# Optimization experiments

Hardware: AMD Instinct MI355X
Metric: run time of the kernel (lower is better)

## Reference

```python
import jax, jax.numpy as jnp
import numpy as np

EMBED = 1024
HEADS = 16
HEAD_DIM = EMBED // HEADS


def setup_inputs() -> dict:
    key = jax.random.key(0)
    ks = jax.random.split(key, 12)
    B, S, E = 2, 2048, EMBED
    scale = 1.0 / np.sqrt(E)
    inp = {
        "query": jax.random.normal(ks[0], (B, S, E), jnp.float32),
        "key": jax.random.normal(ks[1], (B, S, E), jnp.float32),
        "value": jax.random.normal(ks[2], (B, S, E), jnp.float32),
        "Wq": jax.random.normal(ks[3], (E, E), jnp.float32) * scale,
        "bq": jax.random.normal(ks[4], (E,), jnp.float32) * 0.01,
        "Wk": jax.random.normal(ks[5], (E, E), jnp.float32) * scale,
        "bk": jax.random.normal(ks[6], (E,), jnp.float32) * 0.01,
        "Wv": jax.random.normal(ks[7], (E, E), jnp.float32) * scale,
        "bv": jax.random.normal(ks[8], (E,), jnp.float32) * 0.01,
        "Wo": jax.random.normal(ks[9], (E, E), jnp.float32) * scale,
        "bo": jax.random.normal(ks[10], (E,), jnp.float32) * 0.01,
    }
    return inp


def reference(query, key, value, Wq, bq, Wk, bk, Wv, bv, Wo, bo):
    B, Sq, E = query.shape
    Sk = key.shape[1]
    H, D = HEADS, HEAD_DIM
    # QKV projections (torch Linear: x @ W.T + b)
    q = (query @ Wq.T + bq).reshape(B, Sq, H, D)
    k = (key @ Wk.T + bk).reshape(B, Sk, H, D)
    v = (value @ Wv.T + bv).reshape(B, Sk, H, D)
    # energy: [B, H, Sq, Sk]; note scale = 1/sqrt(embed_size), not head_dim
    energy = jnp.einsum("bqhd,bkhd->bhqk", q, k)
    scale = jnp.asarray(E, energy.dtype) ** 0.5
    attn = jax.nn.softmax(energy / scale, axis=-1)
    out = jnp.einsum("bhqk,bkhd->bqhd", attn, v).reshape(B, Sq, E)
    # fc_out (dropout is identity at eval)
    return out @ Wo.T + bo
```

## Files before the change

kernel.cpp:

```cpp
#include <hip/hip_runtime.h>
#include <hip/hip_bf16.h>

typedef __hip_bfloat16 bf16;
typedef short frag8 __attribute__((ext_vector_type(8)));
typedef _Float16 half4 __attribute__((ext_vector_type(4)));
typedef __fp16 fp16x2 __attribute__((ext_vector_type(2)));
typedef float f32x4 __attribute__((ext_vector_type(4)));

typedef __attribute__((address_space(3))) void lds_void;
typedef __attribute__((address_space(1))) const void gbl_void;

__device__ __forceinline__ void gld16(const void* g, void* l) {
  __builtin_amdgcn_global_load_lds((gbl_void*)g, (lds_void*)l, 16, 0, 0);
}

__device__ __forceinline__ unsigned short f2bf(float f) {
  union { float f; unsigned u; } x; x.f = f;
  unsigned r = x.u + 0x7FFFu + ((x.u >> 16) & 1u);
  return (unsigned short)(r >> 16);
}

#define QSCALE 0.0450842200278f
#define MFIX 4.0f

struct CvtArgs {
  const float4* src[7];
  ushort4* dst[7];
  int n4[7];
};
__global__ __launch_bounds__(256) void cvt_all(CvtArgs a) {
  const int t = blockIdx.y;
  const int i = blockIdx.x * 256 + threadIdx.x;
  if (i >= a.n4[t]) return;
  float4 v = a.src[t][i];
  ushort4 o;
  o.x = f2bf(v.x); o.y = f2bf(v.y); o.z = f2bf(v.z); o.w = f2bf(v.w);
  a.dst[t][i] = o;
}

template<int J0>
__device__ __forceinline__ void mfma16(f32x4 (&acc)[8][4], const frag8 (&af)[8], const frag8 (&bf2)[2]) {
  __builtin_amdgcn_s_setprio(1);
  #pragma unroll
  for (int i = 0; i < 8; ++i) {
    #pragma unroll
    for (int j = 0; j < 2; ++j)
      acc[i][J0 + j] = __builtin_amdgcn_mfma_f32_16x16x32_bf16(af[i], bf2[j], acc[i][J0 + j], 0, 0, 0);
  }
  __builtin_amdgcn_s_setprio(0);
}

__global__ __launch_bounds__(512, 2)
void gemm_qkv256(const bf16* __restrict__ A0, const bf16* __restrict__ A1, const bf16* __restrict__ A2,
                 const bf16* __restrict__ W0, const bf16* __restrict__ W1, const bf16* __restrict__ W2,
                 const float* __restrict__ b0, const float* __restrict__ b1, const float* __restrict__ b2,
                 void* __restrict__ o0, void* __restrict__ o1, void* __restrict__ o2) {
  __shared__ __align__(16) bf16 As[2][16384];
  __shared__ __align__(16) bf16 Bs[2][16384];
  const int tid = threadIdx.x;
  const int wave = tid >> 6, lane = tid & 63, quad = lane >> 4, l16 = lane & 15;
  const int wm = wave >> 2, wn = wave & 3;
  const int bn = blockIdx.x, bm = blockIdx.y, z = blockIdx.z;

  const bf16* A = A0; const bf16* W = W0; const float* bias = b0; void* out = o0;
  if (z == 1) { A = A1; W = W1; bias = b1; out = o1; }
  else if (z == 2) { A = A2; W = W2; bias = b2; out = o2; }

  const bf16* Ab = A + (size_t)bm * 256 * 1024;
  const bf16* Wb = W + (size_t)bn * 256 * 1024;
  const int c0_ = tid & 3, r0_ = tid >> 2;
  const int gcp = ((c0_ ^ ((r0_ >> 1) & 3)) << 3);
  const int rc2 = (quad ^ ((l16 >> 1) & 3)) << 3;

  auto stage = [&](const bf16* src, int kt, int kh, bf16* dst) {
    #pragma unroll
    for (int is = 0; is < 2; ++is) {
      const int r = r0_ + is * 128;
      gld16(src + (size_t)r * 1024 + kt * 64 + kh * 32 + gcp,
            (void*)(dst + (is * 512 + tid) * 8));
    }
  };
  auto ldsA = [&](const bf16* ah, frag8 (&af)[8]) {
    #pragma unroll
    for (int i = 0; i < 8; ++i)
      af[i] = *(const frag8*)&ah[(wm * 128 + i * 16 + l16) * 32 + rc2];
  };
  auto ldsB2 = [&](const bf16* bh, int j0, frag8 (&bf2)[2]) {
    #pragma unroll
    for (int j = 0; j < 2; ++j)
      bf2[j] = *(const frag8*)&bh[(wn * 64 + (j0 + j) * 16 + l16) * 32 + rc2];
  };

  f32x4 acc[8][4];
  #pragma unroll
  for (int i = 0; i < 8; ++i)
    #pragma unroll
    for (int j = 0; j < 4; ++j)
      acc[i][j] = (f32x4){0.f, 0.f, 0.f, 0.f};

  stage(Ab, 0, 0, &As[0][0]);
  stage(Wb, 0, 0, &Bs[0][0]);
  stage(Ab, 0, 1, &As[0][8192]);
  stage(Wb, 0, 1, &Bs[0][8192]);
  asm volatile("s_waitcnt vmcnt(0)" ::: "memory");
  __builtin_amdgcn_s_barrier();

  #pragma unroll 2
  for (int t = 0; t < 15; ++t) {
    const int buf = t & 1, nb = buf ^ 1;
    const bf16* a0 = &As[buf][0];    const bf16* a1 = &As[buf][8192];
    const bf16* b0 = &Bs[buf][0];    const bf16* b1 = &Bs[buf][8192];
    frag8 af[8], bf2[2];

    ldsA(a0, af); ldsB2(b0, 0, bf2);
    stage(Ab, t + 1, 0, &As[nb][0]);
    __builtin_amdgcn_s_barrier();
    asm volatile("s_waitcnt lgkmcnt(0)" ::: "memory");
    mfma16<0>(acc, af, bf2);
    __builtin_amdgcn_s_barrier();

    ldsB2(b0, 2, bf2);
    stage(Wb, t + 1, 0, &Bs[nb][0]);
    asm volatile("s_waitcnt vmcnt(4)" ::: "memory");
    __builtin_amdgcn_s_barrier();
    asm volatile("s_waitcnt lgkmcnt(0)" ::: "memory");
    mfma16<2>(acc, af, bf2);
    __builtin_amdgcn_s_barrier();

    ldsA(a1, af); ldsB2(b1, 0, bf2);
    stage(Ab, t + 1, 1, &As[nb][8192]);
    __builtin_amdgcn_s_barrier();
    asm volatile("s_waitcnt lgkmcnt(0)" ::: "memory");
    mfma16<0>(acc, af, bf2);
    __builtin_amdgcn_s_barrier();

    ldsB2(b1, 2, bf2);
    stage(Wb, t + 1, 1, &Bs[nb][8192]);
    asm volatile("s_waitcnt vmcnt(4)" ::: "memory");
    __builtin_amdgcn_s_barrier();
    asm volatile("s_waitcnt lgkmcnt(0)" ::: "memory");
    mfma16<2>(acc, af, bf2);
    __builtin_amdgcn_s_barrier();
  }

  {
    const bf16* a0 = &As[1][0];    const bf16* a1 = &As[1][8192];
    const bf16* b0 = &Bs[1][0];    const bf16* b1 = &Bs[1][8192];
    frag8 af[8], bf2[2];
    ldsA(a0, af); ldsB2(b0, 0, bf2);
    __builtin_amdgcn_s_barrier();
    asm volatile("s_waitcnt lgkmcnt(0)" ::: "memory");
    mfma16<0>(acc, af, bf2);
    ldsB2(b0, 2, bf2);
    asm volatile("s_waitcnt vmcnt(0)" ::: "memory");
    __builtin_amdgcn_s_barrier();
    asm volatile("s_waitcnt lgkmcnt(0)" ::: "memory");
    mfma16<2>(acc, af, bf2);
    ldsA(a1, af); ldsB2(b1, 0, bf2);
    asm volatile("s_waitcnt lgkmcnt(0)" ::: "memory");
    mfma16<0>(acc, af, bf2);
    ldsB2(b1, 2, bf2);
    asm volatile("s_waitcnt lgkmcnt(0)" ::: "memory");
    mfma16<2>(acc, af, bf2);
  }

  #pragma unroll
  for (int j = 0; j < 4; ++j) {
    const int col = bn * 256 + wn * 64 + j * 16 + l16;
    const float bv = bias[col];
    #pragma unroll
    for (int i = 0; i < 8; ++i) {
      #pragma unroll
      for (int r = 0; r < 4; ++r) {
        const int row = bm * 256 + wm * 128 + i * 16 + quad * 4 + r;
        float v = acc[i][j][r] + bv;
        const int b = row >> 11, s = row & 2047;
        const int hh = col >> 6, d = col & 63;
        const size_t bh = (size_t)(b * 16 + hh);
        if (z == 0) {
          v *= QSCALE;
          ((bf16*)out)[(bh * 2048 + s) * 64 + d] = __float2bfloat16(v);
        } else if (z == 1) {
          const int rr = s & 127;
          const size_t addr = bh * 131072 + (size_t)(s >> 7) * 8192 + (size_t)rr * 64
                            + (size_t)(((d >> 3) ^ (rr & 7)) << 3) + (d & 7);
          ((bf16*)out)[addr] = __float2bfloat16(v);
        } else {
          const int kvl = s & 127;
          const size_t addr = bh * 131072 + (size_t)(s >> 7) * 8192 + (size_t)d * 128
                            + (size_t)((((kvl >> 2) ^ (d & 15)) << 2)) + (kvl & 3);
          ((_Float16*)out)[addr] = (_Float16)v;
        }
      }
    }
  }
}

template<int MODE>
__global__ __launch_bounds__(256)
void gemm_bt(const bf16* __restrict__ A0, const bf16* __restrict__ A1, const bf16* __restrict__ A2,
             const bf16* __restrict__ W0, const bf16* __restrict__ W1, const bf16* __restrict__ W2,
             const float* __restrict__ b0, const float* __restrict__ b1, const float* __restrict__ b2,
             void* __restrict__ o0, void* __restrict__ o1, void* __restrict__ o2) {
  constexpr int NK = 1024;
  constexpr int BN = (MODE == 1) ? 128 : 64;
  __shared__ __align__(16) bf16 As[2][128 * 32];
  __shared__ __align__(16) bf16 Bs[2][BN * 32];
  const int tid = threadIdx.x;
  const int wave = tid >> 6, lane = tid & 63, quad = lane >> 4, l16 = lane & 15;
  const int wm = wave >> 1, wn = wave & 1;
  const int bn = blockIdx.x, bm = blockIdx.y;

  const bf16* A = A0; const bf16* W = W0; const float* bias = b0; void* out = o0;

  const bf16* Ab = A + (size_t)bm * 128 * NK;
  const bf16* Wb = W + (size_t)bn * BN * NK;
  const int c0_ = tid & 3, r0_ = tid >> 2;
  const int rc = (quad ^ (l16 & 3)) << 3;

  auto stageA = [&](int k0, int buf) {
    #pragma unroll
    for (int is = 0; is < 2; ++is) {
      const int c = tid + is * 256;
      const int r = r0_ + is * 64;
      const int gc = (c0_ ^ (r & 3)) << 3;
      gld16(Ab + (size_t)r * NK + k0 + gc, (void*)(&As[buf][(size_t)c * 8]));
    }
  };
  auto stageW = [&](int k0, int buf) {
    const int r = r0_;
    const int gc = (c0_ ^ (r & 3)) << 3;
    gld16(Wb + (size_t)r * NK + k0 + gc, (void*)(&Bs[buf][(size_t)tid * 8]));
  };

  f32x4 acc[4][2];
  #pragma unroll
  for (int i = 0; i < 4; ++i)
    #pragma unroll
    for (int j = 0; j < 2; ++j)
      acc[i][j] = (f32x4){0.f, 0.f, 0.f, 0.f};

  stageA(0, 0); stageW(0, 0);
  #pragma unroll 2
  for (int kt = 0; kt < 32; ++kt) {
    __syncthreads();
    if (kt < 31) { stageA((kt + 1) * 32, (kt + 1) & 1); stageW((kt + 1) * 32, (kt + 1) & 1); }
    const bf16* as_ = As[kt & 1];
    const bf16* bs_ = Bs[kt & 1];
    frag8 af[4], bfr[2];
    #pragma unroll
    for (int i = 0; i < 4; ++i)
      af[i] = *(const frag8*)&as_[(wm * 64 + i * 16 + l16) * 32 + rc];
    #pragma unroll
    for (int j = 0; j < 2; ++j)
      bfr[j] = *(const frag8*)&bs_[(wn * 32 + j * 16 + l16) * 32 + rc];
    #pragma unroll
    for (int i = 0; i < 4; ++i)
      #pragma unroll
      for (int j = 0; j < 2; ++j)
        acc[i][j] = __builtin_amdgcn_mfma_f32_16x16x32_bf16(af[i], bfr[j], acc[i][j], 0, 0, 0);
  }

  #pragma unroll
  for (int j = 0; j < 2; ++j) {
    const int col = bn * 64 + wn * 32 + j * 16 + l16;
    const float bv = bias[col];
    #pragma unroll
    for (int i = 0; i < 4; ++i) {
      #pragma unroll
      for (int r = 0; r < 4; ++r) {
        const int row = bm * 128 + wm * 64 + i * 16 + quad * 4 + r;
        ((float*)out)[(size_t)row * 1024 + col] = acc[i][j][r] + bv;
      }
    }
  }
}

__global__ __launch_bounds__(512, 4)
void flash_attn(const bf16* __restrict__ Q, const bf16* __restrict__ K,
                const _Float16* __restrict__ Vt, bf16* __restrict__ ctx) {
  __shared__ __align__(16) char smem[65536];
  bf16* Ks = (bf16*)smem;
  _Float16* Vs = (_Float16*)(smem + 32768);
  const int tid = threadIdx.x;
  const int wave = tid >> 6, lane = tid & 63, quad = lane >> 4, l16 = lane & 15;
  const int qg = wave & 3, kvg = wave >> 2;
  const int bh = blockIdx.x, b = bh >> 4, h = bh & 15;
  const int q0 = blockIdx.y * 128 + qg * 32;
  const bf16* Qb = Q + (size_t)bh * 131072;
  const bf16* Kb = K + (size_t)bh * 131072;
  const _Float16* Vb = Vt + (size_t)bh * 131072;

  frag8 qf[2][2];
  #pragma unroll
  for (int qt = 0; qt < 2; ++qt)
    #pragma unroll
    for (int ks = 0; ks < 2; ++ks)
      qf[qt][ks] = *(const frag8*)(Qb + (size_t)(q0 + qt * 16 + l16) * 64 + ks * 32 + quad * 8);

  f32x4 rsv[2];
  f32x4 o[2][4];
  #pragma unroll
  for (int qt = 0; qt < 2; ++qt) {
    rsv[qt] = (f32x4){0.f, 0.f, 0.f, 0.f};
    #pragma unroll
    for (int dt = 0; dt < 4; ++dt)
      o[qt][dt] = (f32x4){0.f, 0.f, 0.f, 0.f};
  }

  const int xk = l16 & 7;
  const int vd = tid >> 3, vch = (tid & 7) << 3;

  auto stage = [&](int kt, int buf) {
    #pragma unroll
    for (int s = 0; s < 2; ++s) {
      const int g = s * 16 + kt;
      const size_t kgo = (size_t)(g >> 1) * 8192 + (size_t)(g & 1) * 4096;
      gld16(Kb + kgo + (size_t)tid * 8, (void*)(Ks + (s * 2 + buf) * 4096 + tid * 8));
      const size_t vgo = (size_t)(g >> 1) * 8192 + (size_t)(g & 1) * 64;
      gld16(Vb + vgo + (size_t)vd * 128 + vch, (void*)(Vs + (s * 2 + buf) * 4096 + tid * 8));
    }
  };

  stage(0, 0);
  #pragma unroll 2
  for (int kt = 0; kt < 16; ++kt) {
    __syncthreads();
    if (kt < 15) stage(kt + 1, (kt + 1) & 1);
    const bf16* ks_ = Ks + (kvg * 2 + (kt & 1)) * 4096;
    const _Float16* vs_ = Vs + (kvg * 2 + (kt & 1)) * 4096;

    f32x4 s[2][4];
    #pragma unroll
    for (int qt = 0; qt < 2; ++qt)
      #pragma unroll
      for (int jt = 0; jt < 4; ++jt)
        s[qt][jt] = (f32x4){-MFIX, -MFIX, -MFIX, -MFIX};
    #pragma unroll
    for (int ks = 0; ks < 2; ++ks) {
      frag8 kf[4];
      #pragma unroll
      for (int jt = 0; jt < 4; ++jt)
        kf[jt] = *(const frag8*)&ks_[(jt * 16 + l16) * 64 + (((ks * 4 + quad) ^ xk) << 3)];
      __builtin_amdgcn_s_setprio(1);
      #pragma unroll
      for (int qt = 0; qt < 2; ++qt)
        #pragma unroll
        for (int jt = 0; jt < 4; ++jt)
          s[qt][jt] = __builtin_amdgcn_mfma_f32_16x16x32_bf16(kf[jt], qf[qt][ks], s[qt][jt], 0, 0, 0);
      __builtin_amdgcn_s_setprio(0);
    }

    half4 pf[2][4];
    #pragma unroll
    for (int qt = 0; qt < 2; ++qt) {
      #pragma unroll
      for (int jt = 0; jt < 4; ++jt) {
        f32x4 p4;
        #pragma unroll
        for (int r = 0; r < 4; ++r)
          p4[r] = __builtin_amdgcn_exp2f(s[qt][jt][r]);
        rsv[qt] += p4;
        union { fp16x2 h2[2]; half4 h4; } u;
        u.h2[0] = __builtin_amdgcn_cvt_pkrtz(p4[0], p4[1]);
        u.h2[1] = __builtin_amdgcn_cvt_pkrtz(p4[2], p4[3]);
        pf[qt][jt] = u.h4;
      }
    }

    #pragma unroll
    for (int jt = 0; jt < 4; ++jt) {
      half4 vf[4];
      #pragma unroll
      for (int dt = 0; dt < 4; ++dt)
        vf[dt] = *(const half4*)&vs_[(dt * 16 + l16) * 64 + (((jt * 4 + quad) ^ l16) << 2)];
      __builtin_amdgcn_s_setprio(1);
      #pragma unroll
      for (int qt = 0; qt < 2; ++qt)
        #pragma unroll
        for (int dt = 0; dt < 4; ++dt)
          o[qt][dt] = __builtin_amdgcn_mfma_f32_16x16x16f16(vf[dt], pf[qt][jt], o[qt][dt], 0, 0, 0);
      __builtin_amdgcn_s_setprio(0);
    }
  }

  __syncthreads();
  float4* mo = (float4*)smem;
  float*  ml = (float*)(smem + 32768);
  const int mbase = (qg * 64 + lane) * 8;
  if (kvg == 1) {
    #pragma unroll
    for (int qt = 0; qt < 2; ++qt)
      #pragma unroll
      for (int dt = 0; dt < 4; ++dt) {
        const int i = qt * 4 + dt;
        mo[mbase + (i ^ (lane & 7))] = (float4){o[qt][dt][0], o[qt][dt][1], o[qt][dt][2], o[qt][dt][3]};
      }
    ml[(qg * 64 + lane) * 2 + 0] = rsv[0][0] + rsv[0][1] + rsv[0][2] + rsv[0][3];
    ml[(qg * 64 + lane) * 2 + 1] = rsv[1][0] + rsv[1][1] + rsv[1][2] + rsv[1][3];
  }
  __syncthreads();
  if (kvg == 0) {
    #pragma unroll
    for (int qt = 0; qt < 2; ++qt) {
      float l = rsv[qt][0] + rsv[qt][1] + rsv[qt][2] + rsv[qt][3]
              + ml[(qg * 64 + lane) * 2 + qt];
      l += __shfl_xor(l, 16, 64);
      l += __shfl_xor(l, 32, 64);
      const float inv = __builtin_amdgcn_rcpf(l);
      const int q = q0 + qt * 16 + l16;
      #pragma unroll
      for (int dt = 0; dt < 4; ++dt) {
        const int i = qt * 4 + dt;
        const float4 po = mo[mbase + (i ^ (lane & 7))];
        ushort4 w;
        w.x = f2bf((o[qt][dt][0] + po.x) * inv);
        w.y = f2bf((o[qt][dt][1] + po.y) * inv);
        w.z = f2bf((o[qt][dt][2] + po.z) * inv);
        w.w = f2bf((o[qt][dt][3] + po.w) * inv);
        const int d = dt * 16 + quad * 4;
        *(uint2*)&ctx[((size_t)(b * 2048 + q)) * 1024 + h * 64 + d] = *(uint2*)&w;
      }
    }
  }
}

extern "C" void kernel_launch(void* const* d_in, const int* in_sizes, int n_in,
                              void* d_out, int out_size, void* d_ws, size_t ws_size,
                              hipStream_t stream) {
  const float* q_in = (const float*)d_in[0];
  const float* k_in = (const float*)d_in[1];
  const float* v_in = (const float*)d_in[2];
  const float* Wq = (const float*)d_in[3];
  const float* bq = (const float*)d_in[4];
  const float* Wk = (const float*)d_in[5];
  const float* bk = (const float*)d_in[6];
  const float* Wv = (const float*)d_in[7];
  const float* bv = (const float*)d_in[8];
  const float* Wo = (const float*)d_in[9];
  const float* bo = (const float*)d_in[10];

  char* ws = (char*)d_ws;
  const size_t MB = 1024 * 1024;
  bf16* Xq  = (bf16*)(ws + 0 * MB);
  bf16* Xk  = (bf16*)(ws + 8 * MB);
  bf16* Xv  = (bf16*)(ws + 16 * MB);
  bf16* Wqb = (bf16*)(ws + 24 * MB);
  bf16* Wkb = (bf16*)(ws + 26 * MB);
  bf16* Wvb = (bf16*)(ws + 28 * MB);
  bf16* Wob = (bf16*)(ws + 30 * MB);
  bf16* Qw  = (bf16*)(ws + 32 * MB);
  bf16* Kw  = (bf16*)(ws + 40 * MB);
  _Float16* Vtw = (_Float16*)(ws + 48 * MB);
  bf16* Ctx = (bf16*)(ws + 56 * MB);

  {
    CvtArgs a;
    a.src[0] = (const float4*)q_in; a.dst[0] = (ushort4*)Xq;  a.n4[0] = 4194304 / 4;
    a.src[1] = (const float4*)k_in; a.dst[1] = (ushort4*)Xk;  a.n4[1] = 4194304 / 4;
    a.src[2] = (const float4*)v_in; a.dst[2] = (ushort4*)Xv;  a.n4[2] = 4194304 / 4;
    a.src[3] = (const float4*)Wq;   a.dst[3] = (ushort4*)Wqb; a.n4[3] = 1048576 / 4;
    a.src[4] = (const float4*)Wk;   a.dst[4] = (ushort4*)Wkb; a.n4[4] = 1048576 / 4;
    a.src[5] = (const float4*)Wv;   a.dst[5] = (ushort4*)Wvb; a.n4[5] = 1048576 / 4;
    a.src[6] = (const float4*)Wo;   a.dst[6] = (ushort4*)Wob; a.n4[6] = 1048576 / 4;
    cvt_all<<<dim3(4096, 7), 256, 0, stream>>>(a);
  }

  gemm_qkv256<<<dim3(4, 16, 3), 512, 0, stream>>>(Xq, Xk, Xv, Wqb, Wkb, Wvb,
                                                  bq, bk, bv, Qw, Kw, (bf16*)Vtw);
  flash_attn<<<dim3(32, 16), 512, 0, stream>>>(Qw, Kw, Vtw, Ctx);
  gemm_bt<0><<<dim3(16, 32), 256, 0, stream>>>(Ctx, nullptr, nullptr, Wob, nullptr, nullptr,
                                               bo, nullptr, nullptr, d_out, nullptr, nullptr);
}
```

Before: 226.5 us.

## Enlarge flash-attention query tile and reorder QKV GEMM MFMA sub-steps

The flash attention kernel now gives each wave 64 query rows instead of 32 (256 per block, half the grid). Each K/V tile loaded into LDS is therefore reused across more queries, and the merge of the two KV-group partials is done in two rounds so it fits the existing shared buffer. Occupancy drops to 2 blocks per CU because of the larger register footprint. The QKV GEMM inner step is reorganised to load 4 A and 4 B fragments and issue a 4x4 MFMA block per sub-step, rather than 8 A by 2 B, which changes the LDS read pattern and register use. One barrier is also dropped in the epilogue.

```diff
diff --git a/kernel.cpp b/kernel.cpp
--- a/kernel.cpp
+++ b/kernel.cpp
@@ -38,14 +38,14 @@
   a.dst[t][i] = o;
 }
 
-template<int J0>
-__device__ __forceinline__ void mfma16(f32x4 (&acc)[8][4], const frag8 (&af)[8], const frag8 (&bf2)[2]) {
+template<int IH>
+__device__ __forceinline__ void mfma16i(f32x4 (&acc)[8][4], const frag8 (&a4)[4], const frag8 (&b4)[4]) {
   __builtin_amdgcn_s_setprio(1);
   #pragma unroll
-  for (int i = 0; i < 8; ++i) {
-    #pragma unroll
-    for (int j = 0; j < 2; ++j)
-      acc[i][J0 + j] = __builtin_amdgcn_mfma_f32_16x16x32_bf16(af[i], bf2[j], acc[i][J0 + j], 0, 0, 0);
+  for (int i = 0; i < 4; ++i) {
+    #pragma unroll
+    for (int j = 0; j < 4; ++j)
+      acc[IH * 4 + i][j] = __builtin_amdgcn_mfma_f32_16x16x32_bf16(a4[i], b4[j], acc[IH * 4 + i][j], 0, 0, 0);
   }
   __builtin_amdgcn_s_setprio(0);
 }
@@ -80,15 +80,15 @@
             (void*)(dst + (is * 512 + tid) * 8));
     }
   };
-  auto ldsA = [&](const bf16* ah, frag8 (&af)[8]) {
-    #pragma unroll
-    for (int i = 0; i < 8; ++i)
-      af[i] = *(const frag8*)&ah[(wm * 128 + i * 16 + l16) * 32 + rc2];
-  };
-  auto ldsB2 = [&](const bf16* bh, int j0, frag8 (&bf2)[2]) {
-    #pragma unroll
-    for (int j = 0; j < 2; ++j)
-      bf2[j] = *(const frag8*)&bh[(wn * 64 + (j0 + j) * 16 + l16) * 32 + rc2];
+  auto ldsA4 = [&](const bf16* ah, int ih, frag8 (&a4)[4]) {
+    #pragma unroll
+    for (int i = 0; i < 4; ++i)
+      a4[i] = *(const frag8*)&ah[(wm * 128 + ih * 64 + i * 16 + l16) * 32 + rc2];
+  };
+  auto ldsB4 = [&](const bf16* bh, frag8 (&b4)[4]) {
+    #pragma unroll
+    for (int j = 0; j < 4; ++j)
+      b4[j] = *(const frag8*)&bh[(wn * 64 + j * 16 + l16) * 32 + rc2];
   };
 
   f32x4 acc[8][4];
@@ -110,58 +110,57 @@
     const int buf = t & 1, nb = buf ^ 1;
     const bf16* a0 = &As[buf][0];    const bf16* a1 = &As[buf][8192];
     const bf16* b0 = &Bs[buf][0];    const bf16* b1 = &Bs[buf][8192];
-    frag8 af[8], bf2[2];
-
-    ldsA(a0, af); ldsB2(b0, 0, bf2);
+    frag8 af[4], bf4[4];
+
+    ldsA4(a0, 0, af); ldsB4(b0, bf4);
     stage(Ab, t + 1, 0, &As[nb][0]);
     __builtin_amdgcn_s_barrier();
     asm volatile("s_waitcnt lgkmcnt(0)" ::: "memory");
-    mfma16<0>(acc, af, bf2);
-    __builtin_amdgcn_s_barrier();
-
-    ldsB2(b0, 2, bf2);
+    mfma16i<0>(acc, af, bf4);
+    __builtin_amdgcn_s_barrier();
+
+    ldsA4(a0, 1, af);
     stage(Wb, t + 1, 0, &Bs[nb][0]);
     asm volatile("s_waitcnt vmcnt(4)" ::: "memory");
     __builtin_amdgcn_s_barrier();
     asm volatile("s_waitcnt lgkmcnt(0)" ::: "memory");
-    mfma16<2>(acc, af, bf2);
-    __builtin_amdgcn_s_barrier();
-
-    ldsA(a1, af); ldsB2(b1, 0, bf2);
+    mfma16i<1>(acc, af, bf4);
+    __builtin_amdgcn_s_barrier();
+
+    ldsA4(a1, 0, af); ldsB4(b1, bf4);
     stage(Ab, t + 1, 1, &As[nb][8192]);
     __builtin_amdgcn_s_barrier();
     asm volatile("s_waitcnt lgkmcnt(0)" ::: "memory");
-    mfma16<0>(acc, af, bf2);
-    __builtin_amdgcn_s_barrier();
-
-    ldsB2(b1, 2, bf2);
+    mfma16i<0>(acc, af, bf4);
+    __builtin_amdgcn_s_barrier();
+
+    ldsA4(a1, 1, af);
     stage(Wb, t + 1, 1, &Bs[nb][8192]);
     asm volatile("s_waitcnt vmcnt(4)" ::: "memory");
     __builtin_amdgcn_s_barrier();
     asm volatile("s_waitcnt lgkmcnt(0)" ::: "memory");
-    mfma16<2>(acc, af, bf2);
+    mfma16i<1>(acc, af, bf4);
     __builtin_amdgcn_s_barrier();
   }
 
   {
     const bf16* a0 = &As[1][0];    const bf16* a1 = &As[1][8192];
     const bf16* b0 = &Bs[1][0];    const bf16* b1 = &Bs[1][8192];
-    frag8 af[8], bf2[2];
-    ldsA(a0, af); ldsB2(b0, 0, bf2);
-    __builtin_amdgcn_s_barrier();
-    asm volatile("s_waitcnt lgkmcnt(0)" ::: "memory");
-    mfma16<0>(acc, af, bf2);
-    ldsB2(b0, 2, bf2);
+    frag8 af[4], bf4[4];
+    ldsA4(a0, 0, af); ldsB4(b0, bf4);
+    asm volatile("s_waitcnt lgkmcnt(0)" ::: "memory");
+    mfma16i<0>(acc, af, bf4);
+    ldsA4(a0, 1, af);
+    asm volatile("s_waitcnt lgkmcnt(0)" ::: "memory");
+    mfma16i<1>(acc, af, bf4);
     asm volatile("s_waitcnt vmcnt(0)" ::: "memory");
     __builtin_amdgcn_s_barrier();
-    asm volatile("s_waitcnt lgkmcnt(0)" ::: "memory");
-    mfma16<2>(acc, af, bf2);
-    ldsA(a1, af); ldsB2(b1, 0, bf2);
-    asm volatile("s_waitcnt lgkmcnt(0)" ::: "memory");
-    mfma16<0>(acc, af, bf2);
-    ldsB2(b1, 2, bf2);
-    asm volatile("s_waitcnt lgkmcnt(0)" ::: "memory");
-    mfma16<2>(acc, af, bf2);
+    ldsA4(a1, 0, af); ldsB4(b1, bf4);
+    asm volatile("s_waitcnt lgkmcnt(0)" ::: "memory");
+    mfma16i<0>(acc, af, bf4);
+    ldsA4(a1, 1, af);
+    asm volatile("s_waitcnt lgkmcnt(0)" ::: "memory");
+    mfma16i<1>(acc, af, bf4);
   }
 
   #pragma unroll
@@ -276,7 +275,7 @@
   }
 }
 
-__global__ __launch_bounds__(512, 4)
+__global__ __launch_bounds__(512, 2)
 void flash_attn(const bf16* __restrict__ Q, const bf16* __restrict__ K,
                 const _Float16* __restrict__ Vt, bf16* __restrict__ ctx) {
   __shared__ __align__(16) char smem[65536];
@@ -286,22 +285,22 @@
   const int wave = tid >> 6, lane = tid & 63, quad = lane >> 4, l16 = lane & 15;
   const int qg = wave & 3, kvg = wave >> 2;
   const int bh = blockIdx.x, b = bh >> 4, h = bh & 15;
-  const int q0 = blockIdx.y * 128 + qg * 32;
+  const int q0 = blockIdx.y * 256 + qg * 64;
   const bf16* Qb = Q + (size_t)bh * 131072;
   const bf16* Kb = K + (size_t)bh * 131072;
   const _Float16* Vb = Vt + (size_t)bh * 131072;
 
-  frag8 qf[2][2];
-  #pragma unroll
-  for (int qt = 0; qt < 2; ++qt)
+  frag8 qf[4][2];
+  #pragma unroll
+  for (int qt = 0; qt < 4; ++qt)
     #pragma unroll
     for (int ks = 0; ks < 2; ++ks)
       qf[qt][ks] = *(const frag8*)(Qb + (size_t)(q0 + qt * 16 + l16) * 64 + ks * 32 + quad * 8);
 
-  f32x4 rsv[2];
-  f32x4 o[2][4];
-  #pragma unroll
-  for (int qt = 0; qt < 2; ++qt) {
+  f32x4 rsv[4];
+  f32x4 o[4][4];
+  #pragma unroll
+  for (int qt = 0; qt < 4; ++qt) {
     rsv[qt] = (f32x4){0.f, 0.f, 0.f, 0.f};
     #pragma unroll
     for (int dt = 0; dt < 4; ++dt)
@@ -330,9 +329,9 @@
     const bf16* ks_ = Ks + (kvg * 2 + (kt & 1)) * 4096;
     const _Float16* vs_ = Vs + (kvg * 2 + (kt & 1)) * 4096;
 
-    f32x4 s[2][4];
-    #pragma unroll
-    for (int qt = 0; qt < 2; ++qt)
+    f32x4 s[4][4];
+    #pragma unroll
+    for (int qt = 0; qt < 4; ++qt)
       #pragma unroll
       for (int jt = 0; jt < 4; ++jt)
         s[qt][jt] = (f32x4){-MFIX, -MFIX, -MFIX, -MFIX};
@@ -344,16 +343,16 @@
         kf[jt] = *(const frag8*)&ks_[(jt * 16 + l16) * 64 + (((ks * 4 + quad) ^ xk) << 3)];
       __builtin_amdgcn_s_setprio(1);
       #pragma unroll
-      for (int qt = 0; qt < 2; ++qt)
+      for (int qt = 0; qt < 4; ++qt)
         #pragma unroll
         for (int jt = 0; jt < 4; ++jt)
           s[qt][jt] = __builtin_amdgcn_mfma_f32_16x16x32_bf16(kf[jt], qf[qt][ks], s[qt][jt], 0, 0, 0);
       __builtin_amdgcn_s_setprio(0);
     }
 
-    half4 pf[2][4];
-    #pragma unroll
-    for (int qt = 0; qt < 2; ++qt) {
+    half4 pf[4][4];
+    #pragma unroll
+    for (int qt = 0; qt < 4; ++qt) {
       #pragma unroll
       for (int jt = 0; jt < 4; ++jt) {
         f32x4 p4;
@@ -376,7 +375,7 @@
         vf[dt] = *(const half4*)&vs_[(dt * 16 + l16) * 64 + (((jt * 4 + quad) ^ l16) << 2)];
       __builtin_amdgcn_s_setprio(1);
       #pragma unroll
-      for (int qt = 0; qt < 2; ++qt)
+      for (int qt = 0; qt < 4; ++qt)
         #pragma unroll
         for (int dt = 0; dt < 4; ++dt)
           o[qt][dt] = __builtin_amdgcn_mfma_f32_16x16x16f16(vf[dt], pf[qt][jt], o[qt][dt], 0, 0, 0);
@@ -384,42 +383,47 @@
     }
   }
 
-  __syncthreads();
   float4* mo = (float4*)smem;
   float*  ml = (float*)(smem + 32768);
   const int mbase = (qg * 64 + lane) * 8;
-  if (kvg == 1) {
-    #pragma unroll
-    for (int qt = 0; qt < 2; ++qt)
-      #pragma unroll
-      for (int dt = 0; dt < 4; ++dt) {
-        const int i = qt * 4 + dt;
-        mo[mbase + (i ^ (lane & 7))] = (float4){o[qt][dt][0], o[qt][dt][1], o[qt][dt][2], o[qt][dt][3]};
+  #pragma unroll
+  for (int r = 0; r < 2; ++r) {
+    __syncthreads();
+    if (kvg == 1) {
+      #pragma unroll
+      for (int qh = 0; qh < 2; ++qh) {
+        const int qt = r * 2 + qh;
+        #pragma unroll
+        for (int dt = 0; dt < 4; ++dt) {
+          const int i = qh * 4 + dt;
+          mo[mbase + (i ^ (lane & 7))] = (float4){o[qt][dt][0], o[qt][dt][1], o[qt][dt][2], o[qt][dt][3]};
+        }
+        ml[(qg * 64 + lane) * 2 + qh] = rsv[qt][0] + rsv[qt][1] + rsv[qt][2] + rsv[qt][3];
       }
-    ml[(qg * 64 + lane) * 2 + 0] = rsv[0][0] + rsv[0][1] + rsv[0][2] + rsv[0][3];
-    ml[(qg * 64 + lane) * 2 + 1] = rsv[1][0] + rsv[1][1] + rsv[1][2] + rsv[1][3];
-  }
-  __syncthreads();
-  if (kvg == 0) {
-    #pragma unroll
-    for (int qt = 0; qt < 2; ++qt) {
-      float l = rsv[qt][0] + rsv[qt][1] + rsv[qt][2] + rsv[qt][3]
-              + ml[(qg * 64 + lane) * 2 + qt];
-      l += __shfl_xor(l, 16, 64);
-      l += __shfl_xor(l, 32, 64);
-      const float inv = __builtin_amdgcn_rcpf(l);
-      const int q = q0 + qt * 16 + l16;
-      #pragma unroll
-      for (int dt = 0; dt < 4; ++dt) {
-        const int i = qt * 4 + dt;
-        const float4 po = mo[mbase + (i ^ (lane & 7))];
-        ushort4 w;
-        w.x = f2bf((o[qt][dt][0] + po.x) * inv);
-        w.y = f2bf((o[qt][dt][1] + po.y) * inv);
-        w.z = f2bf((o[qt][dt][2] + po.z) * inv);
-        w.w = f2bf((o[qt][dt][3] + po.w) * inv);
-        const int d = dt * 16 + quad * 4;
-        *(uint2*)&ctx[((size_t)(b * 2048 + q)) * 1024 + h * 64 + d] = *(uint2*)&w;
+    }
+    __syncthreads();
+    if (kvg == 0) {
+      #pragma unroll
+      for (int qh = 0; qh < 2; ++qh) {
+        const int qt = r * 2 + qh;
+        float l = rsv[qt][0] + rsv[qt][1] + rsv[qt][2] + rsv[qt][3]
+                + ml[(qg * 64 + lane) * 2 + qh];
+        l += __shfl_xor(l, 16, 64);
+        l += __shfl_xor(l, 32, 64);
+        const float inv = __builtin_amdgcn_rcpf(l);
+        const int q = q0 + qt * 16 + l16;
+        #pragma unroll
+        for (int dt = 0; dt < 4; ++dt) {
+          const int i = qh * 4 + dt;
+          const float4 po = mo[mbase + (i ^ (lane & 7))];
+          ushort4 w;
+          w.x = f2bf((o[qt][dt][0] + po.x) * inv);
+          w.y = f2bf((o[qt][dt][1] + po.y) * inv);
+          w.z = f2bf((o[qt][dt][2] + po.z) * inv);
+          w.w = f2bf((o[qt][dt][3] + po.w) * inv);
+          const int d = dt * 16 + quad * 4;
+          *(uint2*)&ctx[((size_t)(b * 2048 + q)) * 1024 + h * 64 + d] = *(uint2*)&w;
+        }
       }
     }
   }
@@ -468,7 +472,7 @@
 
   gemm_qkv256<<<dim3(4, 16, 3), 512, 0, stream>>>(Xq, Xk, Xv, Wqb, Wkb, Wvb,
                                                   bq, bk, bv, Qw, Kw, (bf16*)Vtw);
-  flash_attn<<<dim3(32, 16), 512, 0, stream>>>(Qw, Kw, Vtw, Ctx);
+  flash_attn<<<dim3(32, 8), 512, 0, stream>>>(Qw, Kw, Vtw, Ctx);
   gemm_bt<0><<<dim3(16, 32), 256, 0, stream>>>(Ctx, nullptr, nullptr, Wob, nullptr, nullptr,
                                                bo, nullptr, nullptr, d_out, nullptr, nullptr);
 }
```

Result: no change. 226.7 us (+0.1%).
